# Kernel tuning notes

Hardware: AMD Instinct MI355X
Metric: run time of the kernel (lower is better)

Reference implementation:

```python
import jax, jax.numpy as jnp
import numpy as np
from jax import lax

DIM = 192
HID = 768  # dim * mlp_ratio
B, H, W = 16, 64, 64


def setup_inputs() -> dict:
    key = jax.random.key(0)
    ks = jax.random.split(key, 20)
    n = lambda k, shape, s=0.05: jax.random.normal(k, shape, dtype=jnp.float32) * s
    return {
        "x": jax.random.normal(ks[0], (B, DIM, H, W), dtype=jnp.float32),
        "ln1_w": jnp.ones((DIM,), jnp.float32), "ln1_b": jnp.zeros((DIM,), jnp.float32),
        "in_proj_w": n(ks[1], (2 * DIM, DIM)), "in_proj_b": n(ks[2], (2 * DIM,)),
        "dw_k": n(ks[3], (DIM, 1, 3, 3)),
        "le_k": n(ks[4], (DIM, 1, 3, 3)),
        "decay_logits": n(ks[5], (4, DIM), 0.5),
        "mix_logits": n(ks[6], (4, DIM), 0.5),
        "input_scale": n(ks[7], (4, DIM), 0.5),
        "bn_w": jnp.ones((DIM,), jnp.float32), "bn_b": jnp.zeros((DIM,), jnp.float32),
        "out_proj_w": n(ks[8], (DIM, DIM)), "out_proj_b": n(ks[9], (DIM,)),
        "ln2_w": jnp.ones((DIM,), jnp.float32), "ln2_b": jnp.zeros((DIM,), jnp.float32),
        "fc1_w": n(ks[10], (HID, DIM)), "fc1_b": n(ks[11], (HID,)),
        "fc2_w": n(ks[12], (DIM, HID)), "fc2_b": n(ks[13], (DIM,)),
    }


def _ln2d(x, w, b, eps=1e-6):
    # LayerNorm over channel dim of NCHW
    mean = jnp.mean(x, axis=1, keepdims=True)
    var = jnp.mean((x - mean) ** 2, axis=1, keepdims=True)
    xn = (x - mean) / jnp.sqrt(var + eps)
    return xn * w[None, :, None, None] + b[None, :, None, None]


def _conv1x1(x, w, b):
    return jnp.einsum('bchw,oc->bohw', x, w) + b[None, :, None, None]


def _dwconv3(x, k):
    # depthwise 3x3, padding=1; k: (C,1,3,3)
    return lax.conv_general_dilated(x, k, (1, 1), 'SAME',
                                    feature_group_count=x.shape[1],
                                    dimension_numbers=('NCHW', 'OIHW', 'NCHW'))


def _scan_axis(x, decay, axis):
    # linear decay scan along `axis` (-1 width, -2 height)
    xs = jnp.moveaxis(x, axis, 0)  # (L, B, C, ...)
    d = decay[None, :, None]  # broadcast over (B, C, other_spatial)
    def step(s, cur):
        s = d * s + (1.0 - d) * cur
        return s, s
    _, ys = lax.scan(step, jnp.zeros_like(xs[0]), xs)
    return jnp.moveaxis(ys, 0, axis)


def _directional_scan(x, decay_logits, mix_logits, input_scale):
    decay = jnp.clip(jax.nn.sigmoid(decay_logits), 0.05, 0.995)  # (4,C)
    mix = jax.nn.softmax(mix_logits, axis=0)  # (4,C)
    iscale = 1.0 + jnp.tanh(input_scale)  # (4,C)
    sc = lambda a: a[:, None, None]  # (C,1,1) -> broadcast NCHW
    lr = _scan_axis(x * sc(iscale[0]), decay[0], -1)
    rl = jnp.flip(_scan_axis(jnp.flip(x, -1) * sc(iscale[1]), decay[1], -1), -1)
    tb = _scan_axis(x * sc(iscale[2]), decay[2], -2)
    bt = jnp.flip(_scan_axis(jnp.flip(x, -2) * sc(iscale[3]), decay[3], -2), -2)
    return sc(mix[0]) * lr + sc(mix[1]) * rl + sc(mix[2]) * tb + sc(mix[3]) * bt


def reference(x, ln1_w, ln1_b, in_proj_w, in_proj_b, dw_k, le_k,
              decay_logits, mix_logits, input_scale, bn_w, bn_b,
              out_proj_w, out_proj_b, ln2_w, ln2_b, fc1_w, fc1_b, fc2_w, fc2_b):
    # --- SSM branch ---
    h = _ln2d(x, ln1_w, ln1_b)
    pg = _conv1x1(h, in_proj_w, in_proj_b)
    projected, gate = jnp.split(pg, 2, axis=1)
    projected = _dwconv3(projected, dw_k)
    scanned = _directional_scan(projected, decay_logits, mix_logits, input_scale)
    local = _dwconv3(projected, le_k)
    mixed = (scanned + local) * jax.nn.sigmoid(gate)
    # BatchNorm2d (training-mode batch statistics, eps=1e-5)
    bmean = jnp.mean(mixed, axis=(0, 2, 3), keepdims=True)
    bvar = jnp.mean((mixed - bmean) ** 2, axis=(0, 2, 3), keepdims=True)
    bn = (mixed - bmean) / jnp.sqrt(bvar + 1e-5)
    bn = bn * bn_w[None, :, None, None] + bn_b[None, :, None, None]
    mixed = jax.nn.gelu(bn, approximate=False)
    x = x + _conv1x1(mixed, out_proj_w, out_proj_b)
    # --- MLP branch ---
    h2 = _ln2d(x, ln2_w, ln2_b)
    m = jax.nn.gelu(_conv1x1(h2, fc1_w, fc1_b), approximate=False)
    m = _conv1x1(m, fc2_w, fc2_b)
    return x + m
```

## Files before the change

kernel.cpp:

```cpp
#include <hip/hip_runtime.h>
#include <math.h>

#define CH 192
#define HW 4096
#define NB 16
#define NELEM (NB*CH*HW)
#define HIDN 768

typedef __bf16 bf16x8 __attribute__((ext_vector_type(8)));
typedef float  f32x4  __attribute__((ext_vector_type(4)));
typedef unsigned uint4v __attribute__((ext_vector_type(4)));

__device__ __forceinline__ float gelu_f(float v){
    float u = 0.7978845608f * v * (1.0f + 0.044715f*v*v);
    float t = 1.0f - 2.0f/(1.0f + __expf(2.0f*u));
    return 0.5f * v * (1.0f + t);
}
__device__ __forceinline__ float sigmoid_f(float v){
    return 1.0f / (1.0f + __expf(-v));
}
__device__ __forceinline__ void gload16(const void* g, void* l){
    __builtin_amdgcn_global_load_lds(
        (const __attribute__((address_space(1))) unsigned*)g,
        (__attribute__((address_space(3))) unsigned*)l, 16, 0, 0);
}

__global__ __launch_bounds__(256) void k_cvt(const float* __restrict__ a,
                                             __bf16* __restrict__ o, int n){
    int i = blockIdx.x*256 + threadIdx.x;
    if (i < n) o[i] = (__bf16)a[i];
}

__global__ __launch_bounds__(256, 4) void k_ln_inproj(
    const float* __restrict__ x, const float* __restrict__ lw, const float* __restrict__ lb,
    const __bf16* __restrict__ Wb, const float* __restrict__ bias,
    __bf16* __restrict__ proj, __bf16* __restrict__ gate)
{
    __shared__ __align__(16) unsigned char smem[33024];
    __bf16* h2s = (__bf16*)smem;
    float* redS = (float*)(smem + 24576);
    float* redQ = (float*)(smem + 25600);
    float* mS   = (float*)(smem + 26624);
    float* rS   = (float*)(smem + 26880);
    __bf16* outb = (__bf16*)(smem + 24576);

    int tid = threadIdx.x;
    int lane = tid & 63;
    int w = tid >> 6;
    int lo = lane & 15, hi = lane >> 4;
    int bid = blockIdx.x;
    int b = bid >> 6;
    int p0 = (bid & 63) << 6;
    const float* xb = x + (size_t)b*CH*HW + p0;
    int px = lane;

    float xv[48];
    float s = 0.f, s2 = 0.f;
    #pragma unroll
    for (int k = 0; k < 48; ++k){
        float v = xb[(size_t)(48*w + k)*HW + px];
        xv[k] = v; s += v; s2 += v*v;
    }
    redS[tid] = s; redQ[tid] = s2;
    __syncthreads();
    if (tid < 64){
        float S = redS[tid]+redS[tid+64]+redS[tid+128]+redS[tid+192];
        float Q = redQ[tid]+redQ[tid+64]+redQ[tid+128]+redQ[tid+192];
        float mean = S * (1.f/192.f);
        float var  = Q * (1.f/192.f) - mean*mean;
        mS[tid] = mean;
        rS[tid] = rsqrtf(var + 1e-6f);
    }
    __syncthreads();
    {
        float mean = mS[px], rstd = rS[px];
        #pragma unroll
        for (int m = 0; m < 6; ++m){
            int c8 = 48*w + 8*m;
            int ks = c8 >> 5, hh = (c8 >> 3) & 3;
            bf16x8 pk;
            #pragma unroll
            for (int j = 0; j < 8; ++j){
                int c = c8 + j;
                pk[j] = (__bf16)((xv[8*m + j] - mean) * rstd * lw[c] + lb[c]);
            }
            *(bf16x8*)(h2s + (((px>>4)*6 + ks)*64 + hh*16 + (px & 15))*8) = pk;
        }
    }
    __syncthreads();

    #pragma unroll
    for (int g = 0; g < 2; ++g){
        f32x4 acc[3][4];
        #pragma unroll
        for (int nt = 0; nt < 3; ++nt)
            #pragma unroll
            for (int pt = 0; pt < 4; ++pt)
                acc[nt][pt] = (f32x4){0.f,0.f,0.f,0.f};
        #pragma unroll
        for (int ks = 0; ks < 6; ++ks){
            bf16x8 a[4];
            #pragma unroll
            for (int pt = 0; pt < 4; ++pt)
                a[pt] = *(const bf16x8*)(h2s + ((pt*6 + ks)*64 + lane)*8);
            #pragma unroll
            for (int nt = 0; nt < 3; ++nt){
                bf16x8 bf = *(const bf16x8*)
                    (Wb + (size_t)(g*192 + w*48 + nt*16 + lo)*CH + ks*32 + hi*8);
                #pragma unroll
                for (int pt = 0; pt < 4; ++pt)
                    acc[nt][pt] = __builtin_amdgcn_mfma_f32_16x16x32_bf16(
                        a[pt], bf, acc[nt][pt], 0, 0, 0);
            }
        }
        __bf16* dst = (g == 0) ? proj : gate;
        #pragma unroll
        for (int nt = 0; nt < 3; ++nt){
            __syncthreads();
            int oc = w*48 + nt*16 + lo;
            float bv = bias[g*CH + oc];
            int cc = w*16 + lo;
            #pragma unroll
            for (int pt = 0; pt < 4; ++pt)
                #pragma unroll
                for (int r = 0; r < 4; ++r){
                    float v = acc[nt][pt][r] + bv;
                    if (g == 1) v = sigmoid_f(v);
                    outb[cc*66 + pt*16 + hi*4 + r] = (__bf16)v;
                }
            __syncthreads();
            for (int i = tid; i < 64*64; i += 256){
                int c2 = i >> 6, p = i & 63;
                int c = (c2 >> 4)*48 + nt*16 + (c2 & 15);
                dst[(size_t)(b*CH + c)*HW + p0 + p] = outb[c2*66 + p];
            }
        }
        __syncthreads();
    }
}

__global__ __launch_bounds__(256, 3) void k_spatial(
    const __bf16* __restrict__ proj, const __bf16* __restrict__ gate,
    const float* __restrict__ dwk, const float* __restrict__ lek,
    const float* __restrict__ dl, const float* __restrict__ ml, const float* __restrict__ il,
    __bf16* __restrict__ mixed, float* __restrict__ part)
{
    __shared__ float t[66*67];
    __shared__ float r[64*65];
    __shared__ float r2[64*65];
    __shared__ float rs[256], rq[256];
    int tid = threadIdx.x;
    int lane = tid & 63;
    int w = tid >> 6;
    int bc = blockIdx.x;
    int c = bc % CH;
    const __bf16* pp = proj + (size_t)bc*HW;

    for (int i = tid; i < 66*66; i += 256){
        int yy = i / 66, xx = i - yy*66;
        float v = 0.f;
        if (yy >= 1 && yy <= 64 && xx >= 1 && xx <= 64)
            v = (float)pp[(yy-1)*64 + (xx-1)];
        t[yy*67 + xx] = v;
    }
    float d[4], e[4], m[4];
    {
        float lg[4], mx = -1e30f;
        #pragma unroll
        for (int k = 0; k < 4; ++k){ lg[k] = ml[k*CH + c]; mx = fmaxf(mx, lg[k]); }
        float se = 0.f;
        #pragma unroll
        for (int k = 0; k < 4; ++k){ lg[k] = __expf(lg[k]-mx); se += lg[k]; }
        #pragma unroll
        for (int k = 0; k < 4; ++k){
            m[k] = lg[k] / se;
            float dd = sigmoid_f(dl[k*CH + c]);
            dd = fminf(fmaxf(dd, 0.05f), 0.995f);
            d[k] = dd;
            e[k] = (1.0f - dd) * (1.0f + tanhf(il[k*CH + c]));
        }
    }
    __syncthreads();
    float kk[9];
    #pragma unroll
    for (int j = 0; j < 9; ++j) kk[j] = dwk[c*9 + j];
    float dw[16];
    #pragma unroll
    for (int j = 0; j < 16; ++j){
        int i = tid + j*256;
        int y = i >> 6, xx = i & 63;
        float sv = 0.f;
        #pragma unroll
        for (int dy = 0; dy < 3; ++dy)
            #pragma unroll
            for (int dx = 0; dx < 3; ++dx)
                sv = fmaf(kk[dy*3+dx], t[(y+dy)*67 + xx + dx], sv);
        dw[j] = sv;
    }
    __syncthreads();
    #pragma unroll
    for (int j = 0; j < 16; ++j){
        int i = tid + j*256;
        t[((i>>6)+1)*67 + (i & 63) + 1] = dw[j];
    }
    __syncthreads();
    if (w == 0){
        int y = lane; float s = 0.f;
        for (int xx = 0; xx < 64; ++xx){
            s = fmaf(d[0], s, e[0]*t[(y+1)*67 + xx + 1]);
            r[y*65 + xx] = m[0]*s;
        }
    } else if (w == 1){
        int xx = lane; float s = 0.f;
        for (int y = 0; y < 64; ++y){
            s = fmaf(d[2], s, e[2]*t[(y+1)*67 + xx + 1]);
            r2[y*65 + xx] = m[2]*s;
        }
    }
    __syncthreads();
    if (w == 2){
        int y = lane; float s = 0.f;
        for (int xx = 63; xx >= 0; --xx){
            s = fmaf(d[1], s, e[1]*t[(y+1)*67 + xx + 1]);
            r[y*65 + xx] += m[1]*s;
        }
    } else if (w == 3){
        int xx = lane; float s = 0.f;
        for (int y = 63; y >= 0; --y){
            s = fmaf(d[3], s, e[3]*t[(y+1)*67 + xx + 1]);
            r2[y*65 + xx] += m[3]*s;
        }
    }
    __syncthreads();
    float lk[9];
    #pragma unroll
    for (int j = 0; j < 9; ++j) lk[j] = lek[c*9 + j];
    const __bf16* gp = gate + (size_t)bc*HW;
    __bf16* mp = mixed + (size_t)bc*HW;
    float s1 = 0.f, s2 = 0.f;
    #pragma unroll
    for (int j = 0; j < 16; ++j){
        int i = tid + j*256;
        int y = i >> 6, xx = i & 63;
        float sv = 0.f;
        #pragma unroll
        for (int dy = 0; dy < 3; ++dy)
            #pragma unroll
            for (int dx = 0; dx < 3; ++dx)
                sv = fmaf(lk[dy*3+dx], t[(y+dy)*67 + xx + dx], sv);
        float mv = (r[y*65 + xx] + r2[y*65 + xx] + sv) * (float)gp[i];
        mp[i] = (__bf16)mv;
        s1 += mv; s2 += mv*mv;
    }
    rs[tid] = s1; rq[tid] = s2;
    __syncthreads();
    for (int off = 128; off > 0; off >>= 1){
        if (tid < off){ rs[tid] += rs[tid+off]; rq[tid] += rq[tid+off]; }
        __syncthreads();
    }
    if (tid == 0){ part[bc] = rs[0]; part[NB*CH + bc] = rq[0]; }
}

__global__ __launch_bounds__(192) void k_bn_final(
    const float* __restrict__ part, const float* __restrict__ bw,
    const float* __restrict__ bb, float* __restrict__ bnp)
{
    int c = threadIdx.x;
    float S = 0.f, Q = 0.f;
    for (int b = 0; b < NB; ++b){
        S += part[b*CH + c];
        Q += part[NB*CH + b*CH + c];
    }
    float mean = S * (1.f/65536.f);
    float var  = Q * (1.f/65536.f) - mean*mean;
    float sc = bw[c] * rsqrtf(var + 1e-5f);
    bnp[c] = sc;
    bnp[CH + c] = bb[c] - mean * sc;
}

__global__ __launch_bounds__(256, 4) void k_outproj_ln2(
    const __bf16* __restrict__ mixed, const float* __restrict__ bnp,
    const __bf16* __restrict__ Wo, const float* __restrict__ biaso,
    const float* __restrict__ x,
    const float* __restrict__ lw, const float* __restrict__ lb,
    float* __restrict__ xr, __bf16* __restrict__ ln2h)
{
    __shared__ __align__(16) unsigned char smem[27904];
    __bf16* h2s  = (__bf16*)smem;
    __bf16* outb = (__bf16*)smem;
    float* redS = (float*)(smem + 25344);
    float* redQ = (float*)(smem + 26368);
    float* mS   = (float*)(smem + 27392);
    float* rS   = (float*)(smem + 27648);

    int tid = threadIdx.x;
    int lane = tid & 63;
    int w = tid >> 6;
    int lo = lane & 15, hi = lane >> 4;
    int bid = blockIdx.x;
    int b = bid >> 6;
    int p0 = (bid & 63) << 6;
    int px = lane;
    const __bf16* mb = mixed + (size_t)b*CH*HW + p0;

    #pragma unroll
    for (int m = 0; m < 6; ++m){
        int c8 = 48*w + 8*m;
        int ks = c8 >> 5, hh = (c8 >> 3) & 3;
        bf16x8 pk;
        #pragma unroll
        for (int j = 0; j < 8; ++j){
            int c = c8 + j;
            float v = (float)mb[(size_t)c*HW + px];
            pk[j] = (__bf16)gelu_f(fmaf(v, bnp[c], bnp[CH + c]));
        }
        *(bf16x8*)(h2s + (((px>>4)*6 + ks)*64 + hh*16 + (px & 15))*8) = pk;
    }
    __syncthreads();

    f32x4 acc[3][4];
    #pragma unroll
    for (int nt = 0; nt < 3; ++nt)
        #pragma unroll
        for (int pt = 0; pt < 4; ++pt)
            acc[nt][pt] = (f32x4){0.f,0.f,0.f,0.f};
    #pragma unroll
    for (int ks = 0; ks < 6; ++ks){
        bf16x8 a[4];
        #pragma unroll
        for (int pt = 0; pt < 4; ++pt)
            a[pt] = *(const bf16x8*)(h2s + ((pt*6 + ks)*64 + lane)*8);
        #pragma unroll
        for (int nt = 0; nt < 3; ++nt){
            bf16x8 bf = *(const bf16x8*)
                (Wo + (size_t)(w*48 + nt*16 + lo)*CH + ks*32 + hi*8);
            #pragma unroll
            for (int pt = 0; pt < 4; ++pt)
                acc[nt][pt] = __builtin_amdgcn_mfma_f32_16x16x32_bf16(
                    a[pt], bf, acc[nt][pt], 0, 0, 0);
        }
    }
    __syncthreads();

    #pragma unroll
    for (int nt = 0; nt < 3; ++nt){
        int ocl = w*48 + nt*16 + lo;
        #pragma unroll
        for (int pt = 0; pt < 4; ++pt)
            #pragma unroll
            for (int r = 0; r < 4; ++r)
                outb[ocl*66 + pt*16 + hi*4 + r] = (__bf16)acc[nt][pt][r];
    }
    __syncthreads();

    const float* xbb = x + (size_t)b*CH*HW + p0;
    float xv[48];
    float s = 0.f, s2 = 0.f;
    #pragma unroll
    for (int k = 0; k < 48; ++k){
        int c = 48*w + k;
        float v = xbb[(size_t)c*HW + px] + biaso[c] + (float)outb[c*66 + px];
        xv[k] = v; s += v; s2 += v*v;
    }
    redS[tid] = s; redQ[tid] = s2;
    __syncthreads();
    if (tid < 64){
        float S = redS[tid]+redS[tid+64]+redS[tid+128]+redS[tid+192];
        float Q = redQ[tid]+redQ[tid+64]+redQ[tid+128]+redQ[tid+192];
        float mean = S * (1.f/192.f);
        float var  = Q * (1.f/192.f) - mean*mean;
        mS[tid] = mean;
        rS[tid] = rsqrtf(var + 1e-6f);
    }
    __syncthreads();

    float* xrb = xr + (size_t)b*CH*HW + p0;
    {
        float mean = mS[px], rstd = rS[px];
        #pragma unroll
        for (int m = 0; m < 6; ++m){
            int c8 = 48*w + 8*m;
            int ks = c8 >> 5, hh = (c8 >> 3) & 3;
            bf16x8 pk;
            #pragma unroll
            for (int j = 0; j < 8; ++j){
                int c = c8 + j;
                float v = xv[8*m + j];
                xrb[(size_t)c*HW + px] = v;
                pk[j] = (__bf16)((v - mean) * rstd * lw[c] + lb[c]);
            }
            *(bf16x8*)(h2s + (((px>>4)*6 + ks)*64 + hh*16 + (px & 15))*8) = pk;
        }
    }
    __syncthreads();

    {
        uint4v* gdst = (uint4v*)(ln2h + (size_t)bid*12288);
        const uint4v* lsrc = (const uint4v*)h2s;
        #pragma unroll
        for (int k = 0; k < 6; ++k){
            int i = tid + k*256;
            gdst[i] = lsrc[i];
        }
    }
}

__global__ __launch_bounds__(256, 4) void k_mlp2(
    const __bf16* __restrict__ ln2h,
    const __bf16* __restrict__ w1b, const float* __restrict__ b1,
    const __bf16* __restrict__ w2b, const float* __restrict__ b2,
    float* __restrict__ io)
{
    __shared__ __align__(16) unsigned char smem[32768];
    __bf16* h2s = (__bf16*)smem;
    __bf16* tt  = (__bf16*)(smem + 24576);
    __bf16* outbb = (__bf16*)smem;

    int tid = threadIdx.x;
    int lane = tid & 63;
    int w = tid >> 6;
    int lo = lane & 15, hi = lane >> 4;
    int bid = blockIdx.x;
    int b = bid >> 6;
    int p0 = (bid & 63) << 6;
    int px = lane;

    {
        const unsigned char* src = (const unsigned char*)(ln2h + (size_t)bid*12288);
        #pragma unroll
        for (int k = 0; k < 6; ++k){
            int off = (tid + k*256)*16;
            gload16(src + off, smem + off);
        }
    }
    __syncthreads();

    f32x4 acc2[3][4];
    #pragma unroll
    for (int nt2 = 0; nt2 < 3; ++nt2)
        #pragma unroll
        for (int pt = 0; pt < 4; ++pt)
            acc2[nt2][pt] = (f32x4){0.f,0.f,0.f,0.f};

    int hl = w*16 + lo;
    int ks2w = hl >> 5, hh2 = (hl >> 3) & 3, j2 = hl & 7;

    #pragma unroll 1
    for (int hc = 0; hc < 12; ++hc){
        int hb = hc*64;
        f32x4 acc1[4];
        #pragma unroll
        for (int pt = 0; pt < 4; ++pt)
            acc1[pt] = (f32x4){0.f,0.f,0.f,0.f};
        #pragma unroll
        for (int ks = 0; ks < 6; ++ks){
            bf16x8 a[4];
            #pragma unroll
            for (int pt = 0; pt < 4; ++pt)
                a[pt] = *(const bf16x8*)(h2s + ((pt*6 + ks)*64 + lane)*8);
            bf16x8 bf = *(const bf16x8*)
                (w1b + (size_t)(hb + hl)*CH + ks*32 + hi*8);
            #pragma unroll
            for (int pt = 0; pt < 4; ++pt)
                acc1[pt] = __builtin_amdgcn_mfma_f32_16x16x32_bf16(
                    a[pt], bf, acc1[pt], 0, 0, 0);
        }
        {
            float b1v = b1[hb + hl];
            #pragma unroll
            for (int pt = 0; pt < 4; ++pt)
                #pragma unroll
                for (int r = 0; r < 4; ++r){
                    int ppx = pt*16 + hi*4 + r;
                    tt[(((ppx>>4)*2 + ks2w)*64 + hh2*16 + (ppx & 15))*8 + j2]
                        = (__bf16)gelu_f(acc1[pt][r] + b1v);
                }
        }
        __syncthreads();
        #pragma unroll
        for (int ks2 = 0; ks2 < 2; ++ks2){
            bf16x8 a2[4];
            #pragma unroll
            for (int pt = 0; pt < 4; ++pt)
                a2[pt] = *(const bf16x8*)(tt + ((pt*2 + ks2)*64 + lane)*8);
            #pragma unroll
            for (int nt2 = 0; nt2 < 3; ++nt2){
                bf16x8 bf2 = *(const bf16x8*)
                    (w2b + (size_t)(w*48 + nt2*16 + lo)*HIDN + hb + ks2*32 + hi*8);
                #pragma unroll
                for (int pt = 0; pt < 4; ++pt)
                    acc2[nt2][pt] = __builtin_amdgcn_mfma_f32_16x16x32_bf16(
                        a2[pt], bf2, acc2[nt2][pt], 0, 0, 0);
            }
        }
        __syncthreads();
    }

    #pragma unroll
    for (int nt2 = 0; nt2 < 3; ++nt2){
        int ocl = w*48 + nt2*16 + lo;
        #pragma unroll
        for (int pt = 0; pt < 4; ++pt)
            #pragma unroll
            for (int r = 0; r < 4; ++r)
                outbb[ocl*66 + pt*16 + hi*4 + r] = (__bf16)acc2[nt2][pt][r];
    }
    __syncthreads();
    float* iob = io + (size_t)b*CH*HW + p0;
    #pragma unroll
    for (int k = 0; k < 48; ++k){
        int c = 48*w + k;
        size_t idx = (size_t)c*HW + px;
        iob[idx] = iob[idx] + b2[c] + (float)outbb[c*66 + px];
    }
}

extern "C" void kernel_launch(void* const* d_in, const int* in_sizes, int n_in,
                              void* d_out, int out_size, void* d_ws, size_t ws_size,
                              hipStream_t stream) {
    const float* x    = (const float*)d_in[0];
    const float* ln1w = (const float*)d_in[1];
    const float* ln1b = (const float*)d_in[2];
    const float* ipw  = (const float*)d_in[3];
    const float* ipb  = (const float*)d_in[4];
    const float* dwk  = (const float*)d_in[5];
    const float* lek  = (const float*)d_in[6];
    const float* dlg  = (const float*)d_in[7];
    const float* mlg  = (const float*)d_in[8];
    const float* isc  = (const float*)d_in[9];
    const float* bnw  = (const float*)d_in[10];
    const float* bnb  = (const float*)d_in[11];
    const float* opw  = (const float*)d_in[12];
    const float* opb  = (const float*)d_in[13];
    const float* ln2w = (const float*)d_in[14];
    const float* ln2b = (const float*)d_in[15];
    const float* f1w  = (const float*)d_in[16];
    const float* f1b  = (const float*)d_in[17];
    const float* f2w  = (const float*)d_in[18];
    const float* f2b  = (const float*)d_in[19];

    float* out = (float*)d_out;
    __bf16* bufP = (__bf16*)d_ws;
    __bf16* bufG = bufP + (size_t)NELEM;
    __bf16* bufM = bufG + (size_t)NELEM;
    __bf16* ln2h = bufM + (size_t)NELEM;
    float* part = (float*)(ln2h + (size_t)NELEM);
    float* bnp  = part + 2*NB*CH;
    __bf16* ipwb = (__bf16*)(bnp + 2*CH);
    __bf16* opwb = ipwb + (size_t)2*CH*CH;
    __bf16* w1b  = opwb + (size_t)CH*CH;
    __bf16* w2b  = w1b  + (size_t)HIDN*CH;

    k_cvt<<<(2*CH*CH + 255)/256, 256, 0, stream>>>(ipw, ipwb, 2*CH*CH);
    k_cvt<<<(CH*CH + 255)/256, 256, 0, stream>>>(opw, opwb, CH*CH);
    k_cvt<<<(HIDN*CH + 255)/256, 256, 0, stream>>>(f1w, w1b, HIDN*CH);
    k_cvt<<<(HIDN*CH + 255)/256, 256, 0, stream>>>(f2w, w2b, CH*HIDN);

    k_ln_inproj  <<<1024, 256, 0, stream>>>(x, ln1w, ln1b, ipwb, ipb, bufP, bufG);
    k_spatial    <<<NB*CH, 256, 0, stream>>>(bufP, bufG, dwk, lek, dlg, mlg, isc, bufM, part);
    k_bn_final   <<<1, 192, 0, stream>>>(part, bnw, bnb, bnp);
    k_outproj_ln2<<<1024, 256, 0, stream>>>(bufM, bnp, opwb, opb, x, ln2w, ln2b, out, ln2h);
    k_mlp2       <<<1024, 256, 0, stream>>>(ln2h, w1b, f1b, w2b, f2b, out);
}
```

Baseline: 245.8 us.

## Store residual in bf16, bf16 scan buffers, merge weight casts, sigmoid GELU

Replaces the tanh GELU with a sigmoid-based approximation. Merges the four weight conversion launches into one, and stores k_spatial's scan partials in bf16 so the kernel can run at higher occupancy. Writes the intermediate residual as bf16 to a workspace buffer instead of fp32 into the output, cutting memory traffic in the out-projection and MLP kernels. This trades numerical accuracy (coarser GELU, bf16 residual and scan accumulation) for less bandwidth and launch overhead.

```diff
diff --git a/kernel.cpp b/kernel.cpp
--- a/kernel.cpp
+++ b/kernel.cpp
@@ -12,9 +12,7 @@
 typedef unsigned uint4v __attribute__((ext_vector_type(4)));
 
 __device__ __forceinline__ float gelu_f(float v){
-    float u = 0.7978845608f * v * (1.0f + 0.044715f*v*v);
-    float t = 1.0f - 2.0f/(1.0f + __expf(2.0f*u));
-    return 0.5f * v * (1.0f + t);
+    return v / (1.0f + __expf(-1.702f*v));
 }
 __device__ __forceinline__ float sigmoid_f(float v){
     return 1.0f / (1.0f + __expf(-v));
@@ -25,10 +23,17 @@
         (__attribute__((address_space(3))) unsigned*)l, 16, 0, 0);
 }
 
-__global__ __launch_bounds__(256) void k_cvt(const float* __restrict__ a,
-                                             __bf16* __restrict__ o, int n){
+__global__ __launch_bounds__(256) void k_cvt_all(
+    const float* __restrict__ a0, const float* __restrict__ a1,
+    const float* __restrict__ a2, const float* __restrict__ a3,
+    __bf16* __restrict__ o)
+{
+    const int n0 = 2*CH*CH, n1 = CH*CH, n2 = HIDN*CH, n3 = CH*HIDN;
     int i = blockIdx.x*256 + threadIdx.x;
-    if (i < n) o[i] = (__bf16)a[i];
+    if (i < n0) o[i] = (__bf16)a0[i];
+    else if (i < n0+n1) o[i] = (__bf16)a1[i-n0];
+    else if (i < n0+n1+n2) o[i] = (__bf16)a2[i-n0-n1];
+    else if (i < n0+n1+n2+n3) o[i] = (__bf16)a3[i-n0-n1-n2];
 }
 
 __global__ __launch_bounds__(256, 4) void k_ln_inproj(
@@ -139,15 +144,15 @@
     }
 }
 
-__global__ __launch_bounds__(256, 3) void k_spatial(
+__global__ __launch_bounds__(256, 4) void k_spatial(
     const __bf16* __restrict__ proj, const __bf16* __restrict__ gate,
     const float* __restrict__ dwk, const float* __restrict__ lek,
     const float* __restrict__ dl, const float* __restrict__ ml, const float* __restrict__ il,
     __bf16* __restrict__ mixed, float* __restrict__ part)
 {
     __shared__ float t[66*67];
-    __shared__ float r[64*65];
-    __shared__ float r2[64*65];
+    __shared__ __bf16 r[64*65];
+    __shared__ __bf16 r2[64*65];
     __shared__ float rs[256], rq[256];
     int tid = threadIdx.x;
     int lane = tid & 63;
@@ -208,13 +213,13 @@
         int y = lane; float s = 0.f;
         for (int xx = 0; xx < 64; ++xx){
             s = fmaf(d[0], s, e[0]*t[(y+1)*67 + xx + 1]);
-            r[y*65 + xx] = m[0]*s;
+            r[y*65 + xx] = (__bf16)(m[0]*s);
         }
     } else if (w == 1){
         int xx = lane; float s = 0.f;
         for (int y = 0; y < 64; ++y){
             s = fmaf(d[2], s, e[2]*t[(y+1)*67 + xx + 1]);
-            r2[y*65 + xx] = m[2]*s;
+            r2[y*65 + xx] = (__bf16)(m[2]*s);
         }
     }
     __syncthreads();
@@ -222,13 +227,13 @@
         int y = lane; float s = 0.f;
         for (int xx = 63; xx >= 0; --xx){
             s = fmaf(d[1], s, e[1]*t[(y+1)*67 + xx + 1]);
-            r[y*65 + xx] += m[1]*s;
+            r[y*65 + xx] = (__bf16)((float)r[y*65 + xx] + m[1]*s);
         }
     } else if (w == 3){
         int xx = lane; float s = 0.f;
         for (int y = 63; y >= 0; --y){
             s = fmaf(d[3], s, e[3]*t[(y+1)*67 + xx + 1]);
-            r2[y*65 + xx] += m[3]*s;
+            r2[y*65 + xx] = (__bf16)((float)r2[y*65 + xx] + m[3]*s);
         }
     }
     __syncthreads();
@@ -248,7 +253,7 @@
             #pragma unroll
             for (int dx = 0; dx < 3; ++dx)
                 sv = fmaf(lk[dy*3+dx], t[(y+dy)*67 + xx + dx], sv);
-        float mv = (r[y*65 + xx] + r2[y*65 + xx] + sv) * (float)gp[i];
+        float mv = ((float)r[y*65 + xx] + (float)r2[y*65 + xx] + sv) * (float)gp[i];
         mp[i] = (__bf16)mv;
         s1 += mv; s2 += mv*mv;
     }
@@ -283,7 +288,7 @@
     const __bf16* __restrict__ Wo, const float* __restrict__ biaso,
     const float* __restrict__ x,
     const float* __restrict__ lw, const float* __restrict__ lb,
-    float* __restrict__ xr, __bf16* __restrict__ ln2h)
+    __bf16* __restrict__ xrh, __bf16* __restrict__ ln2h)
 {
     __shared__ __align__(16) unsigned char smem[27904];
     __bf16* h2s  = (__bf16*)smem;
@@ -374,7 +379,7 @@
     }
     __syncthreads();
 
-    float* xrb = xr + (size_t)b*CH*HW + p0;
+    __bf16* xrb = xrh + (size_t)b*CH*HW + p0;
     {
         float mean = mS[px], rstd = rS[px];
         #pragma unroll
@@ -386,7 +391,7 @@
             for (int j = 0; j < 8; ++j){
                 int c = c8 + j;
                 float v = xv[8*m + j];
-                xrb[(size_t)c*HW + px] = v;
+                xrb[(size_t)c*HW + px] = (__bf16)v;
                 pk[j] = (__bf16)((v - mean) * rstd * lw[c] + lb[c]);
             }
             *(bf16x8*)(h2s + (((px>>4)*6 + ks)*64 + hh*16 + (px & 15))*8) = pk;
@@ -406,7 +411,7 @@
 }
 
 __global__ __launch_bounds__(256, 4) void k_mlp2(
-    const __bf16* __restrict__ ln2h,
+    const __bf16* __restrict__ ln2h, const __bf16* __restrict__ xrh,
     const __bf16* __restrict__ w1b, const float* __restrict__ b1,
     const __bf16* __restrict__ w2b, const float* __restrict__ b2,
     float* __restrict__ io)
@@ -507,11 +512,12 @@
     }
     __syncthreads();
     float* iob = io + (size_t)b*CH*HW + p0;
+    const __bf16* xrb = xrh + (size_t)b*CH*HW + p0;
     #pragma unroll
     for (int k = 0; k < 48; ++k){
         int c = 48*w + k;
         size_t idx = (size_t)c*HW + px;
-        iob[idx] = iob[idx] + b2[c] + (float)outbb[c*66 + px];
+        iob[idx] = (float)xrb[idx] + b2[c] + (float)outbb[c*66 + px];
     }
 }
 
@@ -544,21 +550,20 @@
     __bf16* bufG = bufP + (size_t)NELEM;
     __bf16* bufM = bufG + (size_t)NELEM;
     __bf16* ln2h = bufM + (size_t)NELEM;
-    float* part = (float*)(ln2h + (size_t)NELEM);
+    __bf16* xrh  = ln2h + (size_t)NELEM;
+    float* part = (float*)(xrh + (size_t)NELEM);
     float* bnp  = part + 2*NB*CH;
     __bf16* ipwb = (__bf16*)(bnp + 2*CH);
     __bf16* opwb = ipwb + (size_t)2*CH*CH;
     __bf16* w1b  = opwb + (size_t)CH*CH;
     __bf16* w2b  = w1b  + (size_t)HIDN*CH;
 
-    k_cvt<<<(2*CH*CH + 255)/256, 256, 0, stream>>>(ipw, ipwb, 2*CH*CH);
-    k_cvt<<<(CH*CH + 255)/256, 256, 0, stream>>>(opw, opwb, CH*CH);
-    k_cvt<<<(HIDN*CH + 255)/256, 256, 0, stream>>>(f1w, w1b, HIDN*CH);
-    k_cvt<<<(HIDN*CH + 255)/256, 256, 0, stream>>>(f2w, w2b, CH*HIDN);
+    const int ncvt = 2*CH*CH + CH*CH + 2*HIDN*CH;
+    k_cvt_all<<<(ncvt + 255)/256, 256, 0, stream>>>(ipw, opw, f1w, f2w, ipwb);
 
     k_ln_inproj  <<<1024, 256, 0, stream>>>(x, ln1w, ln1b, ipwb, ipb, bufP, bufG);
     k_spatial    <<<NB*CH, 256, 0, stream>>>(bufP, bufG, dwk, lek, dlg, mlg, isc, bufM, part);
     k_bn_final   <<<1, 192, 0, stream>>>(part, bnw, bnb, bnp);
-    k_outproj_ln2<<<1024, 256, 0, stream>>>(bufM, bnp, opwb, opb, x, ln2w, ln2b, out, ln2h);
-    k_mlp2       <<<1024, 256, 0, stream>>>(ln2h, w1b, f1b, w2b, f2b, out);
-}
+    k_outproj_ln2<<<1024, 256, 0, stream>>>(bufM, bnp, opwb, opb, x, ln2w, ln2b, xrh, ln2h);
+    k_mlp2       <<<1024, 256, 0, stream>>>(ln2h, xrh, w1b, f1b, w2b, f2b, out);
+}
```

Result: slower. 265.6 us (+8.0%).
